# Performance work log

Measured on AMD Instinct MI355X. Metric: run time of the kernel, lower is better.

The kernel has to match this reference:

```python
import jax, jax.numpy as jnp
import numpy as np

NUM_OBJ = 32
OBJ_DIM = 128
MSG_W = 256
FIN_W = 256
BATCH = 256
BN_EPS = 1e-5
NEG_SLOPE = 0.01


def _linear_init(key, fan_in, fan_out):
    # torch nn.Linear default: U(-1/sqrt(fan_in), 1/sqrt(fan_in))
    kw, kb = jax.random.split(key)
    bound = 1.0 / np.sqrt(fan_in)
    w = jax.random.uniform(kw, (fan_out, fan_in), jnp.float32, -bound, bound)
    b = jax.random.uniform(kb, (fan_out,), jnp.float32, -bound, bound)
    return w, b


def setup_inputs() -> dict:
    key = jax.random.key(0)
    ks = jax.random.split(key, 8)
    state = jax.random.normal(ks[0], (BATCH, NUM_OBJ, OBJ_DIM), jnp.float32)
    edges = jax.random.randint(ks[1], (BATCH, NUM_OBJ * NUM_OBJ), 0, 2).astype(jnp.float32)
    msg_w1, msg_b1 = _linear_init(ks[2], OBJ_DIM * 2, MSG_W)
    msg_w2, msg_b2 = _linear_init(ks[3], MSG_W, OBJ_DIM)
    fin_w1, fin_b1 = _linear_init(ks[4], OBJ_DIM * 2, FIN_W)
    fin_w2, fin_b2 = _linear_init(ks[5], FIN_W, OBJ_DIM)
    msg_gamma = jnp.ones((MSG_W,), jnp.float32)
    msg_beta = jnp.zeros((MSG_W,), jnp.float32)
    fin_gamma = jnp.ones((FIN_W,), jnp.float32)
    fin_beta = jnp.zeros((FIN_W,), jnp.float32)
    return {
        "state": state, "edges": edges,
        "msg_w1": msg_w1, "msg_b1": msg_b1, "msg_gamma": msg_gamma, "msg_beta": msg_beta,
        "msg_w2": msg_w2, "msg_b2": msg_b2,
        "fin_w1": fin_w1, "fin_b1": fin_b1, "fin_gamma": fin_gamma, "fin_beta": fin_beta,
        "fin_w2": fin_w2, "fin_b2": fin_b2,
    }


def _batchnorm_train(x, gamma, beta):
    # training-mode BatchNorm1d: batch stats over rows, biased variance
    mean = jnp.mean(x, axis=0)
    var = jnp.mean(jnp.square(x - mean), axis=0)
    return (x - mean) * jax.lax.rsqrt(var + BN_EPS) * gamma + beta


def _mlp(x, w1, b1, gamma, beta, w2, b2):
    h = x @ w1.T + b1
    h = _batchnorm_train(h, gamma, beta)
    h = jnp.where(h >= 0, h, NEG_SLOPE * h)  # LeakyReLU
    return h @ w2.T + b2


def reference(state, edges, msg_w1, msg_b1, msg_gamma, msg_beta, msg_w2, msg_b2,
              fin_w1, fin_b1, fin_gamma, fin_beta, fin_w2, fin_b2):
    B, n, d = state.shape
    src = jnp.repeat(jnp.arange(n), n)   # [n*n]
    tgt = jnp.tile(jnp.arange(n), n)     # [n*n]
    sources = state[:, src]              # [B, n*n, d]
    targets = state[:, tgt]              # [B, n*n, d]
    e = edges[:, :, None]                # [B, n*n, 1]
    need = jnp.concatenate([sources * e, targets * e], axis=2)  # [B, n*n, 2d]
    msgs = _mlp(need.reshape(-1, 2 * d), msg_w1, msg_b1, msg_gamma, msg_beta, msg_w2, msg_b2)
    agg = jnp.sum(msgs.reshape(B, n, n, d), axis=2)  # sum over inner edge group
    sm = jnp.concatenate([state, agg], axis=2).reshape(-1, 2 * d)
    out = _mlp(sm, fin_w1, fin_b1, fin_gamma, fin_beta, fin_w2, fin_b2)
    return out.reshape(B, n, d)
```

## Files before the change

kernel.cpp:

```cpp
#include <hip/hip_runtime.h>

#define NOBJ   32
#define DIM    128
#define HW     256
#define R1     8192
#define NPAIR  262144
#define BN_EPS 1e-5f

typedef unsigned short u16;
typedef unsigned int   u32;
typedef __attribute__((ext_vector_type(8))) short bf16x8;
typedef __attribute__((ext_vector_type(4))) float f32x4;
typedef __attribute__((ext_vector_type(4))) unsigned short u16x4;
typedef __attribute__((ext_vector_type(4))) unsigned int u32x4;

__device__ __forceinline__ u16 f2bf(float f) {
    union { float f; unsigned u; } v; v.f = f;
    unsigned r = v.u + 0x7fffu + ((v.u >> 16) & 1u);
    return (u16)(r >> 16);
}
__device__ __forceinline__ float bf2f(u16 u) {
    union { unsigned u; float f; } v; v.u = ((unsigned)u) << 16; return v.f;
}
__device__ __forceinline__ u16x4 cvt4(float4 v) {
    u16x4 r;
    r[0] = f2bf(v.x); r[1] = f2bf(v.y); r[2] = f2bf(v.z); r[3] = f2bf(v.w);
    return r;
}
__device__ __forceinline__ bf16x8 cvt8_f32(const float* p) {
    f32x4 v0 = *(const f32x4*)p, v1 = *(const f32x4*)(p + 4);
    bf16x8 r;
    #pragma unroll
    for (int k = 0; k < 4; ++k) {
        r[k]     = (short)f2bf(v0[k]);
        r[4 + k] = (short)f2bf(v1[k]);
    }
    return r;
}
__device__ __forceinline__ bf16x8 cvt8_bn(const float* p, const float* a, const float* d) {
    f32x4 v0 = *(const f32x4*)p, v1 = *(const f32x4*)(p + 4);
    f32x4 a0 = *(const f32x4*)a, a1 = *(const f32x4*)(a + 4);
    f32x4 d0 = *(const f32x4*)d, d1 = *(const f32x4*)(d + 4);
    bf16x8 r;
    #pragma unroll
    for (int k = 0; k < 4; ++k) {
        float x0 = fmaf(a0[k], v0[k], d0[k]); x0 = fmaxf(x0, 0.01f * x0);
        float x1 = fmaf(a1[k], v1[k], d1[k]); x1 = fmaxf(x1, 0.01f * x1);
        r[k]     = (short)f2bf(x0);
        r[4 + k] = (short)f2bf(x1);
    }
    return r;
}

__global__ __launch_bounds__(256) void prep_kernel(
    const float* __restrict__ w1, const float4* __restrict__ w2,
    const float4* __restrict__ fw1, const float4* __restrict__ fw2,
    u16x4* __restrict__ W1b, u16x4* __restrict__ W2b,
    u16x4* __restrict__ FW1b, u16x4* __restrict__ FW2b,
    f32x4* __restrict__ sums)
{
    int g = blockIdx.x * 256 + threadIdx.x;
    if (g < 16384) {
        const int o = g * 4, n = o >> 7, k = o & 127;
        const float4 v = *(const float4*)(w1 + (n < 256 ? n * 256 + k
                                                        : (n - 256) * 256 + 128 + k));
        W1b[g] = cvt4(v); return;
    }
    g -= 16384;
    if (g < 8192) { W2b[g] = cvt4(w2[g]); return; }
    g -= 8192;
    if (g < 16384) { FW1b[g] = cvt4(fw1[g]); return; }
    g -= 16384;
    if (g < 8192) { FW2b[g] = cvt4(fw2[g]); return; }
    g -= 8192;
    if (g < 264) { const f32x4 z = {}; sums[g] = z; }
}

__global__ __launch_bounds__(512) void pq_stats(
    const float* __restrict__ state, const u16* __restrict__ W1b,
    const float* __restrict__ edges, const float* __restrict__ b1,
    u16* __restrict__ PQb, u16* __restrict__ Ab, float* __restrict__ EQf,
    float* __restrict__ sums)
{
    __shared__ float Pls[32 * 256];
    __shared__ float Qls[33 * 256];
    __shared__ float redA[8 * 256];
    __shared__ float redB[8 * 256];
    __shared__ u32 masks[32];
    __shared__ __align__(16) unsigned char list8[32 * 32];
    __shared__ float cdf[32];

    const int b    = blockIdx.x;
    const int t    = threadIdx.x;
    const int lane = t & 63;
    const int w    = t >> 6;
    const int lr   = lane & 15;
    const int lk   = (lane >> 4) * 8;
    const int c0   = lane * 4;

    if (t < 256) ((u32*)list8)[t] = 0x20202020u;
    if (t < 64) { const f32x4 z = {}; *(f32x4*)&Qls[32 * 256 + t * 4] = z; }

    const int il_t = t >> 5;
    const int j_t  = t & 31;
    const float ev0 = edges[(size_t)b * 1024 + il_t * 32 + j_t];
    const float ev1 = edges[(size_t)b * 1024 + (il_t + 16) * 32 + j_t];

    const int col0 = w * 64;
    f32x4 acc[2][4] = {};
    #pragma unroll
    for (int ks = 0; ks < 4; ++ks) {
        const int kabs = ks * 32 + lk;
        bf16x8 af[2];
        #pragma unroll
        for (int rf = 0; rf < 2; ++rf)
            af[rf] = cvt8_f32(state + (size_t)(b * 32 + rf * 16 + lr) * 128 + kabs);
        if (w == 0) {
            #pragma unroll
            for (int rf = 0; rf < 2; ++rf)
                *(bf16x8*)(Ab + (size_t)(b * 32 + rf * 16 + lr) * 128 + kabs) = af[rf];
        }
        #pragma unroll
        for (int cf = 0; cf < 4; ++cf) {
            const bf16x8 bf = *(const bf16x8*)(W1b + (size_t)(col0 + cf * 16 + lr) * 128 + kabs);
            #pragma unroll
            for (int rf = 0; rf < 2; ++rf)
                acc[rf][cf] = __builtin_amdgcn_mfma_f32_16x16x32_bf16(af[rf], bf, acc[rf][cf], 0, 0, 0);
        }
    }
    #pragma unroll
    for (int rf = 0; rf < 2; ++rf)
        #pragma unroll
        for (int cf = 0; cf < 4; ++cf) {
            const int col = col0 + cf * 16 + lr;
            #pragma unroll
            for (int r = 0; r < 4; ++r) {
                const int row = rf * 16 + (lane >> 4) * 4 + r;
                const u16 u = f2bf(acc[rf][cf][r]);
                PQb[(size_t)(b * 32 + row) * 512 + col] = u;
                const float fv = bf2f(u);
                if (w < 4) Pls[row * 256 + col]         = fv;
                else       Qls[row * 256 + (col - 256)] = fv;
            }
        }
    __syncthreads();

    {
        const unsigned long long bal0 = __ballot(ev0 != 0.f);
        const u32 m0 = (lane < 32) ? (u32)bal0 : (u32)(bal0 >> 32);
        if (ev0 != 0.f)
            list8[il_t * 32 + __popc(m0 & ((1u << j_t) - 1u))] = (unsigned char)j_t;
        if (j_t == 0) masks[il_t] = m0;
        const unsigned long long bal1 = __ballot(ev1 != 0.f);
        const u32 m1 = (lane < 32) ? (u32)bal1 : (u32)(bal1 >> 32);
        if (ev1 != 0.f)
            list8[(il_t + 16) * 32 + __popc(m1 & ((1u << j_t) - 1u))] = (unsigned char)j_t;
        if (j_t == 0) masks[il_t + 16] = m1;
    }
    __syncthreads();

    if (t < 32) {
        u32 cnt = 0;
        #pragma unroll
        for (int i = 0; i < 32; ++i) cnt += (masks[i] >> t) & 1u;
        cdf[t] = (float)cnt;
    }
    if (t == 0) {
        int tot = 0;
        #pragma unroll
        for (int i = 0; i < 32; ++i) tot += __popc(masks[i]);
        atomicAdd(&sums[512], (float)tot);
    }

    const f32x4 b14 = *(const f32x4*)(b1 + c0);
    f32x4 sumA = {}, sumB = {};

    #pragma unroll
    for (int ii = 0; ii < 4; ++ii) {
        const int il = w * 4 + ii;
        const int n1 = __popc(masks[il]);
        const int npad = (n1 + 3) & ~3;
        const float frd = (float)n1;
        f32x4 eq = {};
        const u32x4 l0 = *(const u32x4*)(list8 + il * 32);
        const u32x4 l1 = *(const u32x4*)(list8 + il * 32 + 16);
        const u32 wbuf[8] = {l0[0], l0[1], l0[2], l0[3], l1[0], l1[1], l1[2], l1[3]};
        #pragma unroll
        for (int wi = 0; wi < 8; ++wi) {
            if (wi * 4 >= npad) break;
            const u32 w4 = wbuf[wi];
            #pragma unroll
            for (int kb = 0; kb < 4; ++kb) {
                const int j = (w4 >> (kb * 8)) & 0xff;
                const f32x4 q = *(const f32x4*)&Qls[j * 256 + c0];
                #pragma unroll
                for (int k = 0; k < 4; ++k) eq[k] += q[k];
            }
        }
        *(f32x4*)(EQf + (size_t)(b * 32 + il) * 256 + c0) = eq;
        const f32x4 p4 = *(const f32x4*)&Pls[il * 256 + c0];
        #pragma unroll
        for (int k = 0; k < 4; ++k) {
            const float pb = p4[k] + b14[k];
            sumA[k] += frd * pb + eq[k];
            sumB[k] = fmaf(frd * pb + 2.f * eq[k], pb, sumB[k]);
        }
    }
    __syncthreads();

    #pragma unroll
    for (int jj = 0; jj < 4; ++jj) {
        const int j = w * 4 + jj;
        const float cdj = cdf[j];
        const f32x4 q = *(const f32x4*)&Qls[j * 256 + c0];
        #pragma unroll
        for (int k = 0; k < 4; ++k) sumB[k] = fmaf(cdj * q[k], q[k], sumB[k]);
    }
    *(f32x4*)&redA[w * 256 + c0] = sumA;
    *(f32x4*)&redB[w * 256 + c0] = sumB;
    __syncthreads();
    if (t < 256) {
        float a = 0.f, bb = 0.f;
        #pragma unroll
        for (int ww = 0; ww < 8; ++ww) {
            a  += redA[ww * 256 + t];
            bb += redB[ww * 256 + t];
        }
        atomicAdd(&sums[t], a);
        atomicAdd(&sums[256 + t], bb);
    }
}

__global__ __launch_bounds__(256) void s_agg_kernel(
    const u16* __restrict__ PQb, const float* __restrict__ edges,
    const float* __restrict__ EQf, const float* __restrict__ sums,
    const float* __restrict__ gamma, const float* __restrict__ beta,
    const float* __restrict__ b1,
    const u16* __restrict__ W2b, const float* __restrict__ b2,
    u16* __restrict__ aggb)
{
    __shared__ float Qls[33 * 256];
    __shared__ u16 Ssb[16 * 256];
    __shared__ __align__(16) unsigned char list8[16 * 32];
    __shared__ int n1s[16];

    const int b    = blockIdx.x;
    const int i0   = blockIdx.y * 16;
    const int t    = threadIdx.x;
    const int lane = t & 63;
    const int w    = t >> 6;
    const int lr   = lane & 15;
    const int lk   = (lane >> 4) * 8;
    const int c0   = lane * 4;

    const float Etot = sums[512];
    const float nz   = (float)NPAIR - Etot;
    const float invN = 1.f / (float)NPAIR;
    const f32x4 s1  = *(const f32x4*)(sums + c0);
    const f32x4 s2  = *(const f32x4*)(sums + 256 + c0);
    const f32x4 g4  = *(const f32x4*)(gamma + c0);
    const f32x4 be4 = *(const f32x4*)(beta + c0);
    const f32x4 b14 = *(const f32x4*)(b1 + c0);
    f32x4 a4, d4, ld4;
    #pragma unroll
    for (int k = 0; k < 4; ++k) {
        const float mean = (s1[k] + nz * b14[k]) * invN;
        const float ms   = (s2[k] + nz * b14[k] * b14[k]) * invN;
        const float var  = fmaf(-mean, mean, ms);
        a4[k]  = g4[k] * rsqrtf(var + BN_EPS);
        d4[k]  = fmaf(b14[k] - mean, a4[k], be4[k]);
        ld4[k] = fmaxf(d4[k], 0.01f * d4[k]);
    }

    #pragma unroll
    for (int it = 0; it < 8; ++it) {
        const int row = w + it * 4;
        const u16x4 qu = *(const u16x4*)(PQb + (size_t)(b * 32 + row) * 512 + 256 + c0);
        f32x4 q;
        #pragma unroll
        for (int k = 0; k < 4; ++k) q[k] = a4[k] * bf2f(qu[k]);
        *(f32x4*)&Qls[row * 256 + c0] = q;
    }
    if (t < 64) { const f32x4 z = {}; *(f32x4*)&Qls[32 * 256 + t * 4] = z; }
    if (t < 128) ((u32*)list8)[t] = 0x20202020u;

    const int il_t = t >> 5;
    const int j_t  = t & 31;
    const float ev0 = edges[(size_t)b * 1024 + (i0 + il_t) * 32 + j_t];
    const float ev1 = edges[(size_t)b * 1024 + (i0 + 8 + il_t) * 32 + j_t];
    __syncthreads();

    {
        const unsigned long long bal0 = __ballot(ev0 != 0.f);
        const u32 m0 = (lane < 32) ? (u32)bal0 : (u32)(bal0 >> 32);
        if (ev0 != 0.f)
            list8[il_t * 32 + __popc(m0 & ((1u << j_t) - 1u))] = (unsigned char)j_t;
        if (j_t == 0) n1s[il_t] = __popc(m0);
        const unsigned long long bal1 = __ballot(ev1 != 0.f);
        const u32 m1 = (lane < 32) ? (u32)bal1 : (u32)(bal1 >> 32);
        if (ev1 != 0.f)
            list8[(8 + il_t) * 32 + __popc(m1 & ((1u << j_t) - 1u))] = (unsigned char)j_t;
        if (j_t == 0) n1s[8 + il_t] = __popc(m1);
    }
    __syncthreads();

    #pragma unroll
    for (int ii = 0; ii < 4; ++ii) {
        const int il = 4 * w + ii;
        const int gi = b * 32 + i0 + il;
        const int n1 = n1s[il];
        const int npad = (n1 + 3) & ~3;
        const float frd = (float)n1;
        const float fz = (float)(32 - n1);
        const float fp = (float)(npad - n1);
        const u16x4 pu = *(const u16x4*)(PQb + (size_t)gi * 512 + c0);
        const f32x4 eq4 = *(const f32x4*)(EQf + (size_t)gi * 256 + c0);
        f32x4 ap, absacc;
        #pragma unroll
        for (int k = 0; k < 4; ++k) {
            ap[k] = fmaf(a4[k], bf2f(pu[k]), d4[k]);
            absacc[k] = -fp * fabsf(ap[k]);
        }
        const u32x4 l0 = *(const u32x4*)(list8 + il * 32);
        const u32x4 l1 = *(const u32x4*)(list8 + il * 32 + 16);
        const u32 wbuf[8] = {l0[0], l0[1], l0[2], l0[3], l1[0], l1[1], l1[2], l1[3]};
        #pragma unroll
        for (int wi = 0; wi < 8; ++wi) {
            if (wi * 4 >= npad) break;
            const u32 w4 = wbuf[wi];
            #pragma unroll
            for (int kb = 0; kb < 4; ++kb) {
                const int j = (w4 >> (kb * 8)) & 0xff;
                const f32x4 q = *(const f32x4*)&Qls[j * 256 + c0];
                #pragma unroll
                for (int k = 0; k < 4; ++k)
                    absacc[k] += fabsf(ap[k] + q[k]);
            }
        }
        u16x4 o;
        #pragma unroll
        for (int k = 0; k < 4; ++k) {
            const float lin = fmaf(frd, ap[k], a4[k] * eq4[k]);
            const float S = fmaf(fz, ld4[k], fmaf(0.505f, lin, 0.495f * absacc[k]));
            o[k] = f2bf(S);
        }
        const int off = (lane * 8) ^ ((il & 7) << 4);
        *(u16x4*)((char*)Ssb + il * 512 + off) = o;
    }
    __syncthreads();

    const int colw = w * 32;
    f32x4 acc2[2] = {};
    #pragma unroll
    for (int ks = 0; ks < 8; ++ks) {
        const int rdoff = (ks * 64 + (lane >> 4) * 16) ^ ((lr & 7) << 4);
        const bf16x8 afr = *(const bf16x8*)((const char*)Ssb + lr * 512 + rdoff);
        #pragma unroll
        for (int cf = 0; cf < 2; ++cf) {
            const bf16x8 bfr = *(const bf16x8*)(W2b + (size_t)(colw + cf * 16 + lr) * 256 + ks * 32 + lk);
            acc2[cf] = __builtin_amdgcn_mfma_f32_16x16x32_bf16(afr, bfr, acc2[cf], 0, 0, 0);
        }
    }
    #pragma unroll
    for (int cf = 0; cf < 2; ++cf) {
        const int col = colw + cf * 16 + lr;
        const float bv = (float)NOBJ * b2[col];
        #pragma unroll
        for (int r = 0; r < 4; ++r) {
            const int rowl = (lane >> 4) * 4 + r;
            aggb[(size_t)(b * 32 + i0 + rowl) * 128 + col] = f2bf(acc2[cf][r] + bv);
        }
    }
}

__global__ __launch_bounds__(256) void h2_gemm(
    const u16* __restrict__ Ab, const u16* __restrict__ aggb,
    const u16* __restrict__ FW1b, const float* __restrict__ fb1,
    float* __restrict__ H2, float* __restrict__ sums2)
{
    __shared__ float sred[64];
    const int lane = threadIdx.x & 63;
    const int wave = threadIdx.x >> 6;
    const int row0 = blockIdx.y * 64 + wave * 16;
    const int col0 = blockIdx.x * 32;
    const int lr = lane & 15;
    const int lk = (lane >> 4) * 8;

    f32x4 acc[2] = {};
    #pragma unroll
    for (int ks = 0; ks < 8; ++ks) {
        const int kabs = ks * 32 + lk;
        const bf16x8 af = (kabs < 128)
            ? *(const bf16x8*)(Ab   + (size_t)(row0 + lr) * 128 + kabs)
            : *(const bf16x8*)(aggb + (size_t)(row0 + lr) * 128 + (kabs - 128));
        #pragma unroll
        for (int cf = 0; cf < 2; ++cf) {
            const bf16x8 bf = *(const bf16x8*)(FW1b + (size_t)(col0 + cf * 16 + lr) * 256 + kabs);
            acc[cf] = __builtin_amdgcn_mfma_f32_16x16x32_bf16(af, bf, acc[cf], 0, 0, 0);
        }
    }

    if (threadIdx.x < 64) sred[threadIdx.x] = 0.f;
    __syncthreads();
    #pragma unroll
    for (int cf = 0; cf < 2; ++cf) {
        const int col = col0 + cf * 16 + lr;
        const float bv = fb1[col];
        float s = 0.f, ss = 0.f;
        #pragma unroll
        for (int r = 0; r < 4; ++r) {
            const int row = row0 + (lane >> 4) * 4 + r;
            const float v = acc[cf][r] + bv;
            H2[(size_t)row * 256 + col] = v;
            s += v;
            ss = fmaf(v, v, ss);
        }
        atomicAdd(&sred[cf * 16 + lr], s);
        atomicAdd(&sred[32 + cf * 16 + lr], ss);
    }
    __syncthreads();
    if (threadIdx.x < 32) {
        atomicAdd(&sums2[col0 + threadIdx.x], sred[threadIdx.x]);
        atomicAdd(&sums2[256 + col0 + threadIdx.x], sred[32 + threadIdx.x]);
    }
}

__global__ __launch_bounds__(256) void out_gemm(
    const float* __restrict__ H2, const u16* __restrict__ FW2b,
    const float* __restrict__ fb2, const float* __restrict__ sums2,
    const float* __restrict__ gamma, const float* __restrict__ beta,
    float* __restrict__ out)
{
    __shared__ float adl[512];
    const int t = threadIdx.x;
    {
        const float invN = 1.f / (float)R1;
        const float mean = sums2[t] * invN;
        const float var  = fmaf(-mean, mean, sums2[256 + t] * invN);
        const float a    = gamma[t] * rsqrtf(var + BN_EPS);
        adl[t]       = a;
        adl[256 + t] = fmaf(-mean, a, beta[t]);
    }
    __syncthreads();

    const int lane = t & 63;
    const int wave = t >> 6;
    const int row0 = blockIdx.y * 64 + wave * 16;
    const int col0 = blockIdx.x * 32;
    const int lr = lane & 15;
    const int lk = (lane >> 4) * 8;

    f32x4 acc[2] = {};
    #pragma unroll
    for (int ks = 0; ks < 8; ++ks) {
        const int kabs = ks * 32 + lk;
        const bf16x8 af = cvt8_bn(H2 + (size_t)(row0 + lr) * 256 + kabs,
                                  adl + kabs, adl + 256 + kabs);
        #pragma unroll
        for (int cf = 0; cf < 2; ++cf) {
            const bf16x8 bf = *(const bf16x8*)(FW2b + (size_t)(col0 + cf * 16 + lr) * 256 + kabs);
            acc[cf] = __builtin_amdgcn_mfma_f32_16x16x32_bf16(af, bf, acc[cf], 0, 0, 0);
        }
    }
    #pragma unroll
    for (int cf = 0; cf < 2; ++cf) {
        const int col = col0 + cf * 16 + lr;
        const float bv = fb2[col];
        #pragma unroll
        for (int r = 0; r < 4; ++r) {
            const int row = row0 + (lane >> 4) * 4 + r;
            out[(size_t)row * 128 + col] = acc[cf][r] + bv;
        }
    }
}

extern "C" void kernel_launch(void* const* d_in, const int* in_sizes, int n_in,
                              void* d_out, int out_size, void* d_ws, size_t ws_size,
                              hipStream_t stream)
{
    const float* state     = (const float*)d_in[0];
    const float* edges     = (const float*)d_in[1];
    const float* msg_w1    = (const float*)d_in[2];
    const float* msg_b1    = (const float*)d_in[3];
    const float* msg_gamma = (const float*)d_in[4];
    const float* msg_beta  = (const float*)d_in[5];
    const float* msg_w2    = (const float*)d_in[6];
    const float* msg_b2    = (const float*)d_in[7];
    const float* fin_w1    = (const float*)d_in[8];
    const float* fin_b1    = (const float*)d_in[9];
    const float* fin_gamma = (const float*)d_in[10];
    const float* fin_beta  = (const float*)d_in[11];
    const float* fin_w2    = (const float*)d_in[12];
    const float* fin_b2    = (const float*)d_in[13];

    char* w = (char*)d_ws;
    u16*   PQb  = (u16*)(w);
    u16*   Ab   = (u16*)(w + 8388608);
    u16*   aggb = (u16*)(w + 10485760);
    float* H2   = (float*)(w + 12582912);
    float* EQf  = (float*)(w + 20971520);
    u16*   W1b  = (u16*)(w + 29360128);
    u16*   W2b  = (u16*)(w + 29491200);
    u16*   FW1b = (u16*)(w + 29556736);
    u16*   FW2b = (u16*)(w + 29687808);
    float* sums = (float*)(w + 29753344);
    float* sums2 = sums + 544;

    prep_kernel<<<195, 256, 0, stream>>>(
        msg_w1, (const float4*)msg_w2, (const float4*)fin_w1, (const float4*)fin_w2,
        (u16x4*)W1b, (u16x4*)W2b, (u16x4*)FW1b, (u16x4*)FW2b, (f32x4*)sums);

    pq_stats<<<256, 512, 0, stream>>>(state, W1b, edges, msg_b1,
                                      PQb, Ab, EQf, sums);

    s_agg_kernel<<<dim3(256, 2), 256, 0, stream>>>(
        PQb, edges, EQf, sums, msg_gamma, msg_beta, msg_b1, W2b, msg_b2, aggb);

    h2_gemm<<<dim3(8, 128), 256, 0, stream>>>(Ab, aggb, FW1b, fin_b1, H2, sums2);

    out_gemm<<<dim3(4, 128), 256, 0, stream>>>(
        H2, FW2b, fin_b2, sums2, fin_gamma, fin_beta, (float*)d_out);
}
```

Measured before the change: 69.39 us.

## Double block sizes in pq_stats and s_agg, store H2 as bf16

Raises pq_stats to 1024 threads and s_agg_kernel to 512 threads, so each wave covers fewer columns and rows. The change drops the fp32 P copy in shared memory and reads P back from global bf16. The H2 intermediate is now stored as bf16 instead of fp32, which halves its write and read traffic between h2_gemm and out_gemm. The larger blocks aim for more parallelism per batch. In exchange there is more register pressure per block, an extra global read for P, and lower precision in H2 before the final batchnorm (its statistics are still accumulated in fp32).

```diff
diff --git a/kernel.cpp b/kernel.cpp
--- a/kernel.cpp
+++ b/kernel.cpp
@@ -37,15 +37,15 @@
     }
     return r;
 }
-__device__ __forceinline__ bf16x8 cvt8_bn(const float* p, const float* a, const float* d) {
-    f32x4 v0 = *(const f32x4*)p, v1 = *(const f32x4*)(p + 4);
+__device__ __forceinline__ bf16x8 cvt8_bn_b(const u16* p, const float* a, const float* d) {
+    u16x4 v0 = *(const u16x4*)p, v1 = *(const u16x4*)(p + 4);
     f32x4 a0 = *(const f32x4*)a, a1 = *(const f32x4*)(a + 4);
     f32x4 d0 = *(const f32x4*)d, d1 = *(const f32x4*)(d + 4);
     bf16x8 r;
     #pragma unroll
     for (int k = 0; k < 4; ++k) {
-        float x0 = fmaf(a0[k], v0[k], d0[k]); x0 = fmaxf(x0, 0.01f * x0);
-        float x1 = fmaf(a1[k], v1[k], d1[k]); x1 = fmaxf(x1, 0.01f * x1);
+        float x0 = fmaf(a0[k], bf2f(v0[k]), d0[k]); x0 = fmaxf(x0, 0.01f * x0);
+        float x1 = fmaf(a1[k], bf2f(v1[k]), d1[k]); x1 = fmaxf(x1, 0.01f * x1);
         r[k]     = (short)f2bf(x0);
         r[4 + k] = (short)f2bf(x1);
     }
@@ -76,16 +76,15 @@
     if (g < 264) { const f32x4 z = {}; sums[g] = z; }
 }
 
-__global__ __launch_bounds__(512) void pq_stats(
+__global__ __launch_bounds__(1024) void pq_stats(
     const float* __restrict__ state, const u16* __restrict__ W1b,
     const float* __restrict__ edges, const float* __restrict__ b1,
     u16* __restrict__ PQb, u16* __restrict__ Ab, float* __restrict__ EQf,
     float* __restrict__ sums)
 {
-    __shared__ float Pls[32 * 256];
     __shared__ float Qls[33 * 256];
-    __shared__ float redA[8 * 256];
-    __shared__ float redB[8 * 256];
+    __shared__ float redA[16 * 256];
+    __shared__ float redB[16 * 256];
     __shared__ u32 masks[32];
     __shared__ __align__(16) unsigned char list8[32 * 32];
     __shared__ float cdf[32];
@@ -101,13 +100,10 @@
     if (t < 256) ((u32*)list8)[t] = 0x20202020u;
     if (t < 64) { const f32x4 z = {}; *(f32x4*)&Qls[32 * 256 + t * 4] = z; }
 
-    const int il_t = t >> 5;
-    const int j_t  = t & 31;
-    const float ev0 = edges[(size_t)b * 1024 + il_t * 32 + j_t];
-    const float ev1 = edges[(size_t)b * 1024 + (il_t + 16) * 32 + j_t];
-
-    const int col0 = w * 64;
-    f32x4 acc[2][4] = {};
+    const float ev = edges[(size_t)b * 1024 + t];
+
+    const int col0 = w * 32;
+    f32x4 acc[2][2] = {};
     #pragma unroll
     for (int ks = 0; ks < 4; ++ks) {
         const int kabs = ks * 32 + lk;
@@ -121,7 +117,7 @@
                 *(bf16x8*)(Ab + (size_t)(b * 32 + rf * 16 + lr) * 128 + kabs) = af[rf];
         }
         #pragma unroll
-        for (int cf = 0; cf < 4; ++cf) {
+        for (int cf = 0; cf < 2; ++cf) {
             const bf16x8 bf = *(const bf16x8*)(W1b + (size_t)(col0 + cf * 16 + lr) * 128 + kabs);
             #pragma unroll
             for (int rf = 0; rf < 2; ++rf)
@@ -131,31 +127,26 @@
     #pragma unroll
     for (int rf = 0; rf < 2; ++rf)
         #pragma unroll
-        for (int cf = 0; cf < 4; ++cf) {
+        for (int cf = 0; cf < 2; ++cf) {
             const int col = col0 + cf * 16 + lr;
             #pragma unroll
             for (int r = 0; r < 4; ++r) {
                 const int row = rf * 16 + (lane >> 4) * 4 + r;
                 const u16 u = f2bf(acc[rf][cf][r]);
                 PQb[(size_t)(b * 32 + row) * 512 + col] = u;
-                const float fv = bf2f(u);
-                if (w < 4) Pls[row * 256 + col]         = fv;
-                else       Qls[row * 256 + (col - 256)] = fv;
+                if (col >= 256) Qls[row * 256 + (col - 256)] = bf2f(u);
             }
         }
     __syncthreads();
 
     {
-        const unsigned long long bal0 = __ballot(ev0 != 0.f);
-        const u32 m0 = (lane < 32) ? (u32)bal0 : (u32)(bal0 >> 32);
-        if (ev0 != 0.f)
-            list8[il_t * 32 + __popc(m0 & ((1u << j_t) - 1u))] = (unsigned char)j_t;
-        if (j_t == 0) masks[il_t] = m0;
-        const unsigned long long bal1 = __ballot(ev1 != 0.f);
-        const u32 m1 = (lane < 32) ? (u32)bal1 : (u32)(bal1 >> 32);
-        if (ev1 != 0.f)
-            list8[(il_t + 16) * 32 + __popc(m1 & ((1u << j_t) - 1u))] = (unsigned char)j_t;
-        if (j_t == 0) masks[il_t + 16] = m1;
+        const int il_t = t >> 5;
+        const int j_t  = t & 31;
+        const unsigned long long bal = __ballot(ev != 0.f);
+        const u32 m32 = (lane < 32) ? (u32)bal : (u32)(bal >> 32);
+        if (ev != 0.f)
+            list8[il_t * 32 + __popc(m32 & ((1u << j_t) - 1u))] = (unsigned char)j_t;
+        if (j_t == 0) masks[il_t] = m32;
     }
     __syncthreads();
 
@@ -176,8 +167,8 @@
     f32x4 sumA = {}, sumB = {};
 
     #pragma unroll
-    for (int ii = 0; ii < 4; ++ii) {
-        const int il = w * 4 + ii;
+    for (int ii = 0; ii < 2; ++ii) {
+        const int il = 2 * w + ii;
         const int n1 = __popc(masks[il]);
         const int npad = (n1 + 3) & ~3;
         const float frd = (float)n1;
@@ -198,10 +189,10 @@
             }
         }
         *(f32x4*)(EQf + (size_t)(b * 32 + il) * 256 + c0) = eq;
-        const f32x4 p4 = *(const f32x4*)&Pls[il * 256 + c0];
+        const u16x4 pu = *(const u16x4*)(PQb + (size_t)(b * 32 + il) * 512 + c0);
         #pragma unroll
         for (int k = 0; k < 4; ++k) {
-            const float pb = p4[k] + b14[k];
+            const float pb = bf2f(pu[k]) + b14[k];
             sumA[k] += frd * pb + eq[k];
             sumB[k] = fmaf(frd * pb + 2.f * eq[k], pb, sumB[k]);
         }
@@ -209,8 +200,8 @@
     __syncthreads();
 
     #pragma unroll
-    for (int jj = 0; jj < 4; ++jj) {
-        const int j = w * 4 + jj;
+    for (int jj = 0; jj < 2; ++jj) {
+        const int j = 2 * w + jj;
         const float cdj = cdf[j];
         const f32x4 q = *(const f32x4*)&Qls[j * 256 + c0];
         #pragma unroll
@@ -222,7 +213,7 @@
     if (t < 256) {
         float a = 0.f, bb = 0.f;
         #pragma unroll
-        for (int ww = 0; ww < 8; ++ww) {
+        for (int ww = 0; ww < 16; ++ww) {
             a  += redA[ww * 256 + t];
             bb += redB[ww * 256 + t];
         }
@@ -231,7 +222,7 @@
     }
 }
 
-__global__ __launch_bounds__(256) void s_agg_kernel(
+__global__ __launch_bounds__(512) void s_agg_kernel(
     const u16* __restrict__ PQb, const float* __restrict__ edges,
     const float* __restrict__ EQf, const float* __restrict__ sums,
     const float* __restrict__ gamma, const float* __restrict__ beta,
@@ -273,8 +264,8 @@
     }
 
     #pragma unroll
-    for (int it = 0; it < 8; ++it) {
-        const int row = w + it * 4;
+    for (int it = 0; it < 4; ++it) {
+        const int row = w + it * 8;
         const u16x4 qu = *(const u16x4*)(PQb + (size_t)(b * 32 + row) * 512 + 256 + c0);
         f32x4 q;
         #pragma unroll
@@ -284,29 +275,23 @@
     if (t < 64) { const f32x4 z = {}; *(f32x4*)&Qls[32 * 256 + t * 4] = z; }
     if (t < 128) ((u32*)list8)[t] = 0x20202020u;
 
-    const int il_t = t >> 5;
-    const int j_t  = t & 31;
-    const float ev0 = edges[(size_t)b * 1024 + (i0 + il_t) * 32 + j_t];
-    const float ev1 = edges[(size_t)b * 1024 + (i0 + 8 + il_t) * 32 + j_t];
+    const float ev = edges[(size_t)b * 1024 + (i0 + (t >> 5)) * 32 + (t & 31)];
     __syncthreads();
 
     {
-        const unsigned long long bal0 = __ballot(ev0 != 0.f);
-        const u32 m0 = (lane < 32) ? (u32)bal0 : (u32)(bal0 >> 32);
-        if (ev0 != 0.f)
-            list8[il_t * 32 + __popc(m0 & ((1u << j_t) - 1u))] = (unsigned char)j_t;
-        if (j_t == 0) n1s[il_t] = __popc(m0);
-        const unsigned long long bal1 = __ballot(ev1 != 0.f);
-        const u32 m1 = (lane < 32) ? (u32)bal1 : (u32)(bal1 >> 32);
-        if (ev1 != 0.f)
-            list8[(8 + il_t) * 32 + __popc(m1 & ((1u << j_t) - 1u))] = (unsigned char)j_t;
-        if (j_t == 0) n1s[8 + il_t] = __popc(m1);
-    }
-    __syncthreads();
-
-    #pragma unroll
-    for (int ii = 0; ii < 4; ++ii) {
-        const int il = 4 * w + ii;
+        const int il_t = t >> 5;
+        const int j_t  = t & 31;
+        const unsigned long long bal = __ballot(ev != 0.f);
+        const u32 m32 = (lane < 32) ? (u32)bal : (u32)(bal >> 32);
+        if (ev != 0.f)
+            list8[il_t * 32 + __popc(m32 & ((1u << j_t) - 1u))] = (unsigned char)j_t;
+        if (j_t == 0) n1s[il_t] = __popc(m32);
+    }
+    __syncthreads();
+
+    #pragma unroll
+    for (int ii = 0; ii < 2; ++ii) {
+        const int il = 2 * w + ii;
         const int gi = b * 32 + i0 + il;
         const int n1 = n1s[il];
         const int npad = (n1 + 3) & ~3;
@@ -349,26 +334,22 @@
     }
     __syncthreads();
 
-    const int colw = w * 32;
-    f32x4 acc2[2] = {};
+    const int colw = w * 16;
+    f32x4 acc2 = {};
     #pragma unroll
     for (int ks = 0; ks < 8; ++ks) {
         const int rdoff = (ks * 64 + (lane >> 4) * 16) ^ ((lr & 7) << 4);
         const bf16x8 afr = *(const bf16x8*)((const char*)Ssb + lr * 512 + rdoff);
-        #pragma unroll
-        for (int cf = 0; cf < 2; ++cf) {
-            const bf16x8 bfr = *(const bf16x8*)(W2b + (size_t)(colw + cf * 16 + lr) * 256 + ks * 32 + lk);
-            acc2[cf] = __builtin_amdgcn_mfma_f32_16x16x32_bf16(afr, bfr, acc2[cf], 0, 0, 0);
-        }
-    }
-    #pragma unroll
-    for (int cf = 0; cf < 2; ++cf) {
-        const int col = colw + cf * 16 + lr;
+        const bf16x8 bfr = *(const bf16x8*)(W2b + (size_t)(colw + lr) * 256 + ks * 32 + lk);
+        acc2 = __builtin_amdgcn_mfma_f32_16x16x32_bf16(afr, bfr, acc2, 0, 0, 0);
+    }
+    {
+        const int col = colw + lr;
         const float bv = (float)NOBJ * b2[col];
         #pragma unroll
         for (int r = 0; r < 4; ++r) {
             const int rowl = (lane >> 4) * 4 + r;
-            aggb[(size_t)(b * 32 + i0 + rowl) * 128 + col] = f2bf(acc2[cf][r] + bv);
+            aggb[(size_t)(b * 32 + i0 + rowl) * 128 + col] = f2bf(acc2[r] + bv);
         }
     }
 }
@@ -376,7 +357,7 @@
 __global__ __launch_bounds__(256) void h2_gemm(
     const u16* __restrict__ Ab, const u16* __restrict__ aggb,
     const u16* __restrict__ FW1b, const float* __restrict__ fb1,
-    float* __restrict__ H2, float* __restrict__ sums2)
+    u16* __restrict__ H2b, float* __restrict__ sums2)
 {
     __shared__ float sred[64];
     const int lane = threadIdx.x & 63;
@@ -411,7 +392,7 @@
         for (int r = 0; r < 4; ++r) {
             const int row = row0 + (lane >> 4) * 4 + r;
             const float v = acc[cf][r] + bv;
-            H2[(size_t)row * 256 + col] = v;
+            H2b[(size_t)row * 256 + col] = f2bf(v);
             s += v;
             ss = fmaf(v, v, ss);
         }
@@ -426,7 +407,7 @@
 }
 
 __global__ __launch_bounds__(256) void out_gemm(
-    const float* __restrict__ H2, const u16* __restrict__ FW2b,
+    const u16* __restrict__ H2b, const u16* __restrict__ FW2b,
     const float* __restrict__ fb2, const float* __restrict__ sums2,
     const float* __restrict__ gamma, const float* __restrict__ beta,
     float* __restrict__ out)
@@ -454,8 +435,8 @@
     #pragma unroll
     for (int ks = 0; ks < 8; ++ks) {
         const int kabs = ks * 32 + lk;
-        const bf16x8 af = cvt8_bn(H2 + (size_t)(row0 + lr) * 256 + kabs,
-                                  adl + kabs, adl + 256 + kabs);
+        const bf16x8 af = cvt8_bn_b(H2b + (size_t)(row0 + lr) * 256 + kabs,
+                                    adl + kabs, adl + 256 + kabs);
         #pragma unroll
         for (int cf = 0; cf < 2; ++cf) {
             const bf16x8 bf = *(const bf16x8*)(FW2b + (size_t)(col0 + cf * 16 + lr) * 256 + kabs);
@@ -497,27 +478,27 @@
     u16*   PQb  = (u16*)(w);
     u16*   Ab   = (u16*)(w + 8388608);
     u16*   aggb = (u16*)(w + 10485760);
-    float* H2   = (float*)(w + 12582912);
-    float* EQf  = (float*)(w + 20971520);
-    u16*   W1b  = (u16*)(w + 29360128);
-    u16*   W2b  = (u16*)(w + 29491200);
-    u16*   FW1b = (u16*)(w + 29556736);
-    u16*   FW2b = (u16*)(w + 29687808);
-    float* sums = (float*)(w + 29753344);
+    u16*   H2b  = (u16*)(w + 12582912);
+    float* EQf  = (float*)(w + 16777216);
+    u16*   W1b  = (u16*)(w + 25165824);
+    u16*   W2b  = (u16*)(w + 25296896);
+    u16*   FW1b = (u16*)(w + 25362432);
+    u16*   FW2b = (u16*)(w + 25493504);
+    float* sums = (float*)(w + 25559040);
     float* sums2 = sums + 544;
 
     prep_kernel<<<195, 256, 0, stream>>>(
         msg_w1, (const float4*)msg_w2, (const float4*)fin_w1, (const float4*)fin_w2,
         (u16x4*)W1b, (u16x4*)W2b, (u16x4*)FW1b, (u16x4*)FW2b, (f32x4*)sums);
 
-    pq_stats<<<256, 512, 0, stream>>>(state, W1b, edges, msg_b1,
-                                      PQb, Ab, EQf, sums);
-
-    s_agg_kernel<<<dim3(256, 2), 256, 0, stream>>>(
+    pq_stats<<<256, 1024, 0, stream>>>(state, W1b, edges, msg_b1,
+                                       PQb, Ab, EQf, sums);
+
+    s_agg_kernel<<<dim3(256, 2), 512, 0, stream>>>(
         PQb, edges, EQf, sums, msg_gamma, msg_beta, msg_b1, W2b, msg_b2, aggb);
 
-    h2_gemm<<<dim3(8, 128), 256, 0, stream>>>(Ab, aggb, FW1b, fin_b1, H2, sums2);
+    h2_gemm<<<dim3(8, 128), 256, 0, stream>>>(Ab, aggb, FW1b, fin_b1, H2b, sums2);
 
     out_gemm<<<dim3(4, 128), 256, 0, stream>>>(
-        H2, FW2b, fin_b2, sums2, fin_gamma, fin_beta, (float*)d_out);
-}
+        H2b, FW2b, fin_b2, sums2, fin_gamma, fin_beta, (float*)d_out);
+}
```

New measurement: 69.09 us. Within noise of the previous version (-0.4%).
